# Kernel tuning notes

Hardware: AMD Instinct MI355X
Metric: run time of the kernel (lower is better)

The kernel has to match this reference:

```python
import jax, jax.numpy as jnp
import numpy as np

TOP_K = 8
CAP_FACTOR = 2  # expert capacity = CAP_FACTOR * T*K/E; generous so random routing drops ~nothing


def setup_inputs() -> dict:
    key = jax.random.key(0)
    ks = jax.random.split(key, 6)
    T, H, I, E = 4096, 1536, 768, 64
    return {
        "hidden_states": jax.random.normal(ks[0], (T, H), jnp.float32),
        "gate_w": jax.random.normal(ks[1], (E, H), jnp.float32) * 0.02,
        "routing_bias": jax.random.normal(ks[2], (E,), jnp.float32) * 0.02,
        "w_gate": jax.random.normal(ks[3], (E, I, H), jnp.float32) * 0.02,
        "w_up": jax.random.normal(ks[4], (E, I, H), jnp.float32) * 0.02,
        "w_down": jax.random.normal(ks[5], (E, H, I), jnp.float32) * 0.02,
        "num_global_tokens": 4096,
        "max_num_tokens_per_gpu": 4096,
    }


def _moe(hidden_states, gate_w, routing_bias, w_gate, w_up, w_down):
    T, H = hidden_states.shape
    E = gate_w.shape[0]
    K = TOP_K
    C = (CAP_FACTOR * T * K) // E  # expert capacity

    # router gemm in fp32 (matches fp32 gate / fp32_router_gemm)
    logits = hidden_states.astype(jnp.float32) @ gate_w.T           # [T, E]
    scores = jax.nn.sigmoid(logits)                                  # MiniMax2 sigmoid routing
    sel = scores + routing_bias[None, :]                             # correction bias only for selection
    _, idx = jax.lax.top_k(sel, K)                                   # [T, K]
    w = jnp.take_along_axis(scores, idx, axis=1)                     # weights from raw scores
    w = w / jnp.sum(w, axis=1, keepdims=True)                        # renormalize; routed_scaling_factor = 1.0

    # dispatch: position of each (token, k) row within its expert
    eids = idx.reshape(-1)                                           # [T*K]
    onehot = (eids[:, None] == jnp.arange(E)[None, :]).astype(jnp.int32)
    pos = jnp.take_along_axis(jnp.cumsum(onehot, axis=0) - 1, eids[:, None], axis=1)[:, 0]
    keep = pos < C
    posc = jnp.where(keep, pos, 0)
    x_rows = jnp.repeat(hidden_states, K, axis=0)                    # [T*K, H]
    xd = jnp.zeros((E, C, H), hidden_states.dtype).at[eids, posc].add(
        x_rows * keep[:, None].astype(hidden_states.dtype))         # [E, C, H]

    # grouped expert SwiGLU GEMMs
    g = jnp.einsum('ech,eih->eci', xd, w_gate)                       # [E, C, I]
    u = jnp.einsum('ech,eih->eci', xd, w_up)
    h = jax.nn.silu(g) * u
    y = jnp.einsum('eci,ehi->ech', h, w_down)                        # [E, C, H]

    # combine
    y_rows = y[eids, posc] * keep[:, None].astype(y.dtype)           # [T*K, H]
    out = jnp.sum(y_rows.reshape(T, K, H) * w.reshape(T, K, 1).astype(y.dtype), axis=1)
    return out.astype(hidden_states.dtype)


def reference(hidden_states, gate_w, routing_bias, w_gate, w_up, w_down,
              num_global_tokens, max_num_tokens_per_gpu):
    # num_global_tokens / max_num_tokens_per_gpu are distributed bookkeeping; no effect on math.
    return _moe(hidden_states, gate_w, routing_bias, w_gate, w_up, w_down)
```

## Files before the change

kernel.cpp:

```cpp
#include <hip/hip_runtime.h>
#include <hip/hip_bf16.h>
#include <math.h>

#define TTOK 4096
#define HD   1536
#define IDIM 768
#define NE   64
#define KSEL 8
#define CAP  1024
#define ECAP (NE * CAP)

typedef unsigned int uint32;
typedef __bf16 bf16;
typedef __attribute__((ext_vector_type(8))) __bf16 bf16x8;
typedef __attribute__((ext_vector_type(4))) __bf16 bf16x4;
typedef __attribute__((ext_vector_type(4))) float f32x4;

__global__ __launch_bounds__(256) void k_cast(const float* __restrict__ x, bf16* __restrict__ xb) {
    int i = (blockIdx.x * 256 + threadIdx.x) * 8;
    float4 a = *(const float4*)(x + i);
    float4 b = *(const float4*)(x + i + 4);
    bf16x8 o;
    o[0] = (bf16)a.x; o[1] = (bf16)a.y; o[2] = (bf16)a.z; o[3] = (bf16)a.w;
    o[4] = (bf16)b.x; o[5] = (bf16)b.y; o[6] = (bf16)b.z; o[7] = (bf16)b.w;
    *(bf16x8*)(xb + i) = o;
}

__global__ __launch_bounds__(256) void k_router(const float* __restrict__ x, const float* __restrict__ gw,
                                                double* __restrict__ logits) {
    __shared__ float Xt[8 * HD];
    int t0 = blockIdx.x * 8;
    int tid = threadIdx.x;
    {
        const float4* src = (const float4*)(x + (size_t)t0 * HD);
        float4* dst = (float4*)Xt;
        for (int u = tid; u < 8 * HD / 4; u += 256) dst[u] = src[u];
    }
    __syncthreads();
    int tr = tid >> 5;
    int er = (tid & 31) * 2;
    const float* xr = Xt + tr * HD;
    const float* g0 = gw + (size_t)er * HD;
    const float* g1 = g0 + HD;
    double c0 = 0.0, c1 = 0.0;
    for (int k = 0; k < HD; k += 4) {
        float4 a  = *(const float4*)(xr + k);
        float4 b0 = *(const float4*)(g0 + k);
        float4 b1 = *(const float4*)(g1 + k);
        c0 += (double)a.x * b0.x + (double)a.y * b0.y + (double)a.z * b0.z + (double)a.w * b0.w;
        c1 += (double)a.x * b1.x + (double)a.y * b1.y + (double)a.z * b1.z + (double)a.w * b1.w;
    }
    double* lp = logits + (size_t)(t0 + tr) * NE + er;
    lp[0] = c0; lp[1] = c1;
}

__global__ __launch_bounds__(64) void k_topk(const double* __restrict__ logits, const float* __restrict__ bias,
                                             float* __restrict__ wv, uint32* __restrict__ rowtok,
                                             uint32* __restrict__ tkof, int* __restrict__ cnt) {
    int t = blockIdx.x, lane = threadIdx.x;
    double lg = logits[(size_t)t * NE + lane];
    double sig = 1.0 / (1.0 + exp(-lg));
    double sel = sig + (double)bias[lane];
    double mysig = sig;
    double wsum = 0.0;
    int my_e = -1; double my_s = 0.0;
    for (int k = 0; k < KSEL; ++k) {
        double v = sel; int ei = lane;
        #pragma unroll
        for (int off = 32; off > 0; off >>= 1) {
            double ov = __shfl_down(v, off);
            int    oi = __shfl_down(ei, off);
            if (ov > v || (ov == v && oi < ei)) { v = ov; ei = oi; }
        }
        ei = __shfl(ei, 0);
        double sw = __shfl(mysig, ei);
        wsum += sw;
        if (lane == k) { my_e = ei; my_s = sw; }
        if (lane == ei) sel = -1.0e300;
    }
    if (lane < KSEL) {
        float w = (float)(my_s / wsum);
        int tk = t * KSEL + lane;
        int pos = atomicAdd(cnt + my_e, 1);
        if (pos < CAP) {
            rowtok[my_e * CAP + pos] = (uint32)t;
            tkof  [my_e * CAP + pos] = (uint32)tk;
            wv[tk] = w;
        } else {
            wv[tk] = 0.0f;
        }
    }
}

__global__ __launch_bounds__(256) void k_gemm1(const bf16* __restrict__ xb,
        const float* __restrict__ wg, const float* __restrict__ wu,
        const uint32* __restrict__ rowtok, const int* __restrict__ cnt,
        bf16* __restrict__ hc) {
    int id = blockIdx.x;
    int G  = ((id >> 6) << 3) | (id & 7);
    int mt = (id >> 3) & 7;
    int e  = G / 12, nt = G % 12;
    int n_rows = cnt[e];
    if (mt * 128 >= n_rows) return;

    __shared__ __align__(16) bf16 As[4 * 128 * 8];
    __shared__ __align__(16) bf16 Bg[4 * 64 * 8];
    __shared__ __align__(16) bf16 Bu[4 * 64 * 8];

    int tid = threadIdx.x;
    int am  = tid >> 2;
    int akc = tid & 3;
    int r0 = mt * 128 + am, r1 = r0 + 64;
    uint32 tok0 = (r0 < n_rows) ? rowtok[e * CAP + r0] : 0u;
    uint32 tok1 = (r1 < n_rows) ? rowtok[e * CAP + r1] : 0u;
    const bf16* a0p = xb + (size_t)tok0 * HD + akc * 8;
    const bf16* a1p = xb + (size_t)tok1 * HD + akc * 8;
    const float* wgp = wg + ((size_t)e * IDIM + nt * 64 + am) * HD + akc * 8;
    const float* wup = wu + ((size_t)e * IDIM + nt * 64 + am) * HD + akc * 8;

    int wave = tid >> 6, lane = tid & 63;
    int wm = wave & 1, wn = wave >> 1;
    int q = lane >> 4, r = lane & 15;

    f32x4 zero = {0.f, 0.f, 0.f, 0.f};
    f32x4 accg[4][2], accu[4][2];
    #pragma unroll
    for (int s = 0; s < 4; ++s)
        #pragma unroll
        for (int t2 = 0; t2 < 2; ++t2) { accg[s][t2] = zero; accu[s][t2] = zero; }

    bf16* asw0 = As + ((akc * 128) + am) * 8;
    bf16* asw1 = As + ((akc * 128) + am + 64) * 8;
    bf16* bgw  = Bg + ((akc * 64) + am) * 8;
    bf16* buw  = Bu + ((akc * 64) + am) * 8;

    for (int k0 = 0; k0 < HD; k0 += 32) {
        uint4 va0 = *(const uint4*)(a0p + k0);
        uint4 va1 = *(const uint4*)(a1p + k0);
        float4 gA = *(const float4*)(wgp + k0);
        float4 gB = *(const float4*)(wgp + k0 + 4);
        float4 uA = *(const float4*)(wup + k0);
        float4 uB = *(const float4*)(wup + k0 + 4);
        __syncthreads();
        *(uint4*)asw0 = va0;
        *(uint4*)asw1 = va1;
        bf16x8 pg, pu;
        pg[0]=(bf16)gA.x; pg[1]=(bf16)gA.y; pg[2]=(bf16)gA.z; pg[3]=(bf16)gA.w;
        pg[4]=(bf16)gB.x; pg[5]=(bf16)gB.y; pg[6]=(bf16)gB.z; pg[7]=(bf16)gB.w;
        pu[0]=(bf16)uA.x; pu[1]=(bf16)uA.y; pu[2]=(bf16)uA.z; pu[3]=(bf16)uA.w;
        pu[4]=(bf16)uB.x; pu[5]=(bf16)uB.y; pu[6]=(bf16)uB.z; pu[7]=(bf16)uB.w;
        *(bf16x8*)bgw = pg;
        *(bf16x8*)buw = pu;
        __syncthreads();
        bf16x8 af[4], bgf[2], buf2[2];
        #pragma unroll
        for (int s = 0; s < 4; ++s)
            af[s] = *(const bf16x8*)(As + (q * 128 + wm * 64 + s * 16 + r) * 8);
        #pragma unroll
        for (int t2 = 0; t2 < 2; ++t2) {
            bgf[t2]  = *(const bf16x8*)(Bg + (q * 64 + wn * 32 + t2 * 16 + r) * 8);
            buf2[t2] = *(const bf16x8*)(Bu + (q * 64 + wn * 32 + t2 * 16 + r) * 8);
        }
        #pragma unroll
        for (int s = 0; s < 4; ++s)
            #pragma unroll
            for (int t2 = 0; t2 < 2; ++t2) {
                accg[s][t2] = __builtin_amdgcn_mfma_f32_16x16x32_bf16(af[s], bgf[t2],  accg[s][t2], 0, 0, 0);
                accu[s][t2] = __builtin_amdgcn_mfma_f32_16x16x32_bf16(af[s], buf2[t2], accu[s][t2], 0, 0, 0);
            }
    }
    size_t rowbase = (size_t)e * CAP + mt * 128;
    #pragma unroll
    for (int s = 0; s < 4; ++s)
        #pragma unroll
        for (int t2 = 0; t2 < 2; ++t2)
            #pragma unroll
            for (int rg = 0; rg < 4; ++rg) {
                int row = wm * 64 + s * 16 + q * 4 + rg;
                int col = nt * 64 + wn * 32 + t2 * 16 + r;
                float g = accg[s][t2][rg], u = accu[s][t2][rg];
                float h = g / (1.f + __expf(-g)) * u;
                hc[(rowbase + row) * (size_t)IDIM + col] = (bf16)h;
            }
}

__global__ __launch_bounds__(256) void k_gemm2(const bf16* __restrict__ hc,
        const float* __restrict__ wd, const uint32* __restrict__ tkof,
        const int* __restrict__ cnt, bf16* __restrict__ yw) {
    int id = blockIdx.x;
    int G  = ((id >> 6) << 3) | (id & 7);
    int mt = (id >> 3) & 7;
    int e  = G / 12, nt = G % 12;
    int n_rows = cnt[e];
    if (mt * 128 >= n_rows) return;

    __shared__ __align__(16) bf16 As[4 * 128 * 8];
    __shared__ __align__(16) bf16 Bs[4 * 128 * 8];

    int tid = threadIdx.x;
    int am = tid >> 2, akc = tid & 3;
    const bf16*  a0p = hc + ((size_t)e * CAP + mt * 128 + am) * IDIM + akc * 8;
    const bf16*  a1p = a0p + (size_t)64 * IDIM;
    const float* b0p = wd + ((size_t)e * HD + nt * 128 + am) * IDIM + akc * 8;
    const float* b1p = b0p + (size_t)64 * IDIM;

    int wave = tid >> 6, lane = tid & 63;
    int wm = wave & 1, wn = wave >> 1;
    int q = lane >> 4, r = lane & 15;

    f32x4 zero = {0.f, 0.f, 0.f, 0.f};
    f32x4 acc[4][4];
    #pragma unroll
    for (int s = 0; s < 4; ++s)
        #pragma unroll
        for (int t2 = 0; t2 < 4; ++t2) acc[s][t2] = zero;

    bf16* asw0 = As + (akc * 128 + am) * 8;
    bf16* asw1 = As + (akc * 128 + am + 64) * 8;
    bf16* bsw0 = Bs + (akc * 128 + am) * 8;
    bf16* bsw1 = Bs + (akc * 128 + am + 64) * 8;

    for (int k0 = 0; k0 < IDIM; k0 += 32) {
        uint4 va0 = *(const uint4*)(a0p + k0);
        uint4 va1 = *(const uint4*)(a1p + k0);
        float4 cA = *(const float4*)(b0p + k0);
        float4 cB = *(const float4*)(b0p + k0 + 4);
        float4 dA = *(const float4*)(b1p + k0);
        float4 dB = *(const float4*)(b1p + k0 + 4);
        __syncthreads();
        *(uint4*)asw0 = va0;
        *(uint4*)asw1 = va1;
        bf16x8 p0, p1;
        p0[0]=(bf16)cA.x; p0[1]=(bf16)cA.y; p0[2]=(bf16)cA.z; p0[3]=(bf16)cA.w;
        p0[4]=(bf16)cB.x; p0[5]=(bf16)cB.y; p0[6]=(bf16)cB.z; p0[7]=(bf16)cB.w;
        p1[0]=(bf16)dA.x; p1[1]=(bf16)dA.y; p1[2]=(bf16)dA.z; p1[3]=(bf16)dA.w;
        p1[4]=(bf16)dB.x; p1[5]=(bf16)dB.y; p1[6]=(bf16)dB.z; p1[7]=(bf16)dB.w;
        *(bf16x8*)bsw0 = p0;
        *(bf16x8*)bsw1 = p1;
        __syncthreads();
        bf16x8 af[4], bf4[4];
        #pragma unroll
        for (int s = 0; s < 4; ++s)
            af[s] = *(const bf16x8*)(As + (q * 128 + wm * 64 + s * 16 + r) * 8);
        #pragma unroll
        for (int t2 = 0; t2 < 4; ++t2)
            bf4[t2] = *(const bf16x8*)(Bs + (q * 128 + wn * 64 + t2 * 16 + r) * 8);
        #pragma unroll
        for (int s = 0; s < 4; ++s)
            #pragma unroll
            for (int t2 = 0; t2 < 4; ++t2)
                acc[s][t2] = __builtin_amdgcn_mfma_f32_16x16x32_bf16(af[s], bf4[t2], acc[s][t2], 0, 0, 0);
    }
    uint32 tkx[4][4];
    #pragma unroll
    for (int s = 0; s < 4; ++s)
        #pragma unroll
        for (int rg = 0; rg < 4; ++rg) {
            int row = mt * 128 + wm * 64 + s * 16 + q * 4 + rg;
            tkx[s][rg] = (row < n_rows) ? tkof[e * CAP + row] : 0xFFFFFFFFu;
        }
    #pragma unroll
    for (int s = 0; s < 4; ++s)
        #pragma unroll
        for (int t2 = 0; t2 < 4; ++t2)
            #pragma unroll
            for (int rg = 0; rg < 4; ++rg) {
                if (tkx[s][rg] != 0xFFFFFFFFu) {
                    int col = nt * 128 + wn * 64 + t2 * 16 + r;
                    yw[(size_t)tkx[s][rg] * HD + col] = (bf16)acc[s][t2][rg];
                }
            }
}

__global__ __launch_bounds__(256) void k_combine(const bf16* __restrict__ yw,
        const float* __restrict__ wv, float* __restrict__ out) {
    int t = blockIdx.x, tid = threadIdx.x;
    __shared__ float w8[KSEL];
    if (tid < KSEL) w8[tid] = wv[t * KSEL + tid];
    __syncthreads();
    for (int c0 = tid * 4; c0 < HD; c0 += 1024) {
        float a0 = 0.f, a1 = 0.f, a2 = 0.f, a3 = 0.f;
        #pragma unroll
        for (int k = 0; k < KSEL; ++k) {
            bf16x4 v = *(const bf16x4*)(yw + ((size_t)(t * KSEL + k)) * HD + c0);
            float wk = w8[k];
            a0 += wk * (float)v[0];
            a1 += wk * (float)v[1];
            a2 += wk * (float)v[2];
            a3 += wk * (float)v[3];
        }
        float4 o = {a0, a1, a2, a3};
        *(float4*)(out + (size_t)t * HD + c0) = o;
    }
}

extern "C" void kernel_launch(void* const* d_in, const int* in_sizes, int n_in,
                              void* d_out, int out_size, void* d_ws, size_t ws_size,
                              hipStream_t stream) {
    const float* x  = (const float*)d_in[0];
    const float* gw = (const float*)d_in[1];
    const float* rb = (const float*)d_in[2];
    const float* wg = (const float*)d_in[3];
    const float* wu = (const float*)d_in[4];
    const float* wd = (const float*)d_in[5];
    float* out = (float*)d_out;

    char* ws = (char*)d_ws;
    size_t off = 0;
    auto alloc = [&](size_t bytes) -> void* {
        off = (off + 255) & ~(size_t)255;
        void* p = ws + off;
        off += bytes;
        return p;
    };
    bf16*   xb     = (bf16*)   alloc((size_t)TTOK * HD * 2);
    double* logits = (double*) alloc((size_t)TTOK * NE * 8);
    float*  wv     = (float*)  alloc((size_t)TTOK * KSEL * 4);
    uint32* rowtok = (uint32*) alloc((size_t)ECAP * 4);
    uint32* tkof   = (uint32*) alloc((size_t)ECAP * 4);
    int*    cnt    = (int*)    alloc(256);
    bf16*   hc     = (bf16*)   alloc((size_t)ECAP * IDIM * 2);
    bf16*   yw     = (bf16*)   alloc((size_t)TTOK * KSEL * HD * 2);
    (void)ws_size; (void)in_sizes; (void)n_in; (void)out_size; (void)rb;

    hipMemsetAsync(cnt, 0, 256, stream);
    k_cast   <<<TTOK * HD / 2048, 256, 0, stream>>>(x, xb);
    k_router <<<TTOK / 8,         256, 0, stream>>>(x, gw, logits);
    k_topk   <<<TTOK,             64,  0, stream>>>(logits, rb, wv, rowtok, tkof, cnt);
    k_gemm1  <<<6144,             256, 0, stream>>>(xb, wg, wu, rowtok, cnt, hc);
    k_gemm2  <<<6144,             256, 0, stream>>>(hc, wd, tkof, cnt, yw);
    k_combine<<<TTOK,             256, 0, stream>>>(yw, wv, out);
}
```

Before: 1.473 ms.

## Pre-cast expert weights to bf16 and stage GEMM tiles via global_load_lds

Adds a single cast kernel that converts all three expert weight tensors, plus the activations, to bf16 in workspace every call. Both grouped GEMMs then load bf16 tiles straight into LDS with global_load_lds in an MFMA-fragment-friendly layout, instead of loading fp32 into registers, converting and storing to LDS. This removes per-tile conversion and the register round-trip. The cost is an extra full pass over roughly 900MB of fp32 weights on every call, which may outweigh the savings, plus a second barrier per k-step. yw now aliases the wgb buffer.

```diff
diff --git a/kernel.cpp b/kernel.cpp
--- a/kernel.cpp
+++ b/kernel.cpp
@@ -16,14 +16,26 @@
 typedef __attribute__((ext_vector_type(4))) __bf16 bf16x4;
 typedef __attribute__((ext_vector_type(4))) float f32x4;
 
-__global__ __launch_bounds__(256) void k_cast(const float* __restrict__ x, bf16* __restrict__ xb) {
-    int i = (blockIdx.x * 256 + threadIdx.x) * 8;
-    float4 a = *(const float4*)(x + i);
-    float4 b = *(const float4*)(x + i + 4);
+#define GLD16(g, l) __builtin_amdgcn_global_load_lds( \
+    (const __attribute__((address_space(1))) void*)(g), \
+    (__attribute__((address_space(3))) void*)(l), 16, 0, 0)
+
+__global__ __launch_bounds__(256) void k_castall(const float* __restrict__ wg, const float* __restrict__ wu,
+        const float* __restrict__ wd, const float* __restrict__ x,
+        bf16* __restrict__ wgb, bf16* __restrict__ wub, bf16* __restrict__ wdb, bf16* __restrict__ xb) {
+    int b = blockIdx.x;
+    const float* src; bf16* dst; int base;
+    if      (b <  36864) { src = wg; dst = wgb; base = b; }
+    else if (b <  73728) { src = wu; dst = wub; base = b - 36864; }
+    else if (b < 110592) { src = wd; dst = wdb; base = b - 73728; }
+    else                 { src = x;  dst = xb;  base = b - 110592; }
+    size_t i = ((size_t)base * 256 + threadIdx.x) * 8;
+    float4 a = *(const float4*)(src + i);
+    float4 c = *(const float4*)(src + i + 4);
     bf16x8 o;
     o[0] = (bf16)a.x; o[1] = (bf16)a.y; o[2] = (bf16)a.z; o[3] = (bf16)a.w;
-    o[4] = (bf16)b.x; o[5] = (bf16)b.y; o[6] = (bf16)b.z; o[7] = (bf16)b.w;
-    *(bf16x8*)(xb + i) = o;
+    o[4] = (bf16)c.x; o[5] = (bf16)c.y; o[6] = (bf16)c.z; o[7] = (bf16)c.w;
+    *(bf16x8*)(dst + i) = o;
 }
 
 __global__ __launch_bounds__(256) void k_router(const float* __restrict__ x, const float* __restrict__ gw,
@@ -93,7 +105,7 @@
 }
 
 __global__ __launch_bounds__(256) void k_gemm1(const bf16* __restrict__ xb,
-        const float* __restrict__ wg, const float* __restrict__ wu,
+        const bf16* __restrict__ wgb, const bf16* __restrict__ wub,
         const uint32* __restrict__ rowtok, const int* __restrict__ cnt,
         bf16* __restrict__ hc) {
     int id = blockIdx.x;
@@ -103,24 +115,29 @@
     int n_rows = cnt[e];
     if (mt * 128 >= n_rows) return;
 
-    __shared__ __align__(16) bf16 As[4 * 128 * 8];
-    __shared__ __align__(16) bf16 Bg[4 * 64 * 8];
-    __shared__ __align__(16) bf16 Bu[4 * 64 * 8];
-
-    int tid = threadIdx.x;
-    int am  = tid >> 2;
-    int akc = tid & 3;
-    int r0 = mt * 128 + am, r1 = r0 + 64;
+    __shared__ __align__(16) bf16 As[128 * 32];
+    __shared__ __align__(16) bf16 Bg[64 * 32];
+    __shared__ __align__(16) bf16 Bu[64 * 32];
+
+    int tid = threadIdx.x, wave = tid >> 6, lane = tid & 63;
+    int kc = lane >> 4, mr = lane & 15;
+
+    int g0 = wave * 2, g1 = g0 + 1;
+    int r0 = mt * 128 + g0 * 16 + mr, r1 = mt * 128 + g1 * 16 + mr;
     uint32 tok0 = (r0 < n_rows) ? rowtok[e * CAP + r0] : 0u;
     uint32 tok1 = (r1 < n_rows) ? rowtok[e * CAP + r1] : 0u;
-    const bf16* a0p = xb + (size_t)tok0 * HD + akc * 8;
-    const bf16* a1p = xb + (size_t)tok1 * HD + akc * 8;
-    const float* wgp = wg + ((size_t)e * IDIM + nt * 64 + am) * HD + akc * 8;
-    const float* wup = wu + ((size_t)e * IDIM + nt * 64 + am) * HD + akc * 8;
-
-    int wave = tid >> 6, lane = tid & 63;
+    const bf16* ga0 = xb + (size_t)tok0 * HD + kc * 8;
+    const bf16* ga1 = xb + (size_t)tok1 * HD + kc * 8;
+    const bf16* gbg = wgb + ((size_t)e * IDIM + nt * 64 + wave * 16 + mr) * HD + kc * 8;
+    const bf16* gbu = wub + ((size_t)e * IDIM + nt * 64 + wave * 16 + mr) * HD + kc * 8;
+
+    bf16* lA0 = As + g0 * 512;
+    bf16* lA1 = As + g1 * 512;
+    bf16* lBg = Bg + wave * 512;
+    bf16* lBu = Bu + wave * 512;
+
     int wm = wave & 1, wn = wave >> 1;
-    int q = lane >> 4, r = lane & 15;
+    int r = lane & 15, q = lane >> 4;
 
     f32x4 zero = {0.f, 0.f, 0.f, 0.f};
     f32x4 accg[4][2], accu[4][2];
@@ -129,37 +146,20 @@
         #pragma unroll
         for (int t2 = 0; t2 < 2; ++t2) { accg[s][t2] = zero; accu[s][t2] = zero; }
 
-    bf16* asw0 = As + ((akc * 128) + am) * 8;
-    bf16* asw1 = As + ((akc * 128) + am + 64) * 8;
-    bf16* bgw  = Bg + ((akc * 64) + am) * 8;
-    bf16* buw  = Bu + ((akc * 64) + am) * 8;
-
     for (int k0 = 0; k0 < HD; k0 += 32) {
-        uint4 va0 = *(const uint4*)(a0p + k0);
-        uint4 va1 = *(const uint4*)(a1p + k0);
-        float4 gA = *(const float4*)(wgp + k0);
-        float4 gB = *(const float4*)(wgp + k0 + 4);
-        float4 uA = *(const float4*)(wup + k0);
-        float4 uB = *(const float4*)(wup + k0 + 4);
-        __syncthreads();
-        *(uint4*)asw0 = va0;
-        *(uint4*)asw1 = va1;
-        bf16x8 pg, pu;
-        pg[0]=(bf16)gA.x; pg[1]=(bf16)gA.y; pg[2]=(bf16)gA.z; pg[3]=(bf16)gA.w;
-        pg[4]=(bf16)gB.x; pg[5]=(bf16)gB.y; pg[6]=(bf16)gB.z; pg[7]=(bf16)gB.w;
-        pu[0]=(bf16)uA.x; pu[1]=(bf16)uA.y; pu[2]=(bf16)uA.z; pu[3]=(bf16)uA.w;
-        pu[4]=(bf16)uB.x; pu[5]=(bf16)uB.y; pu[6]=(bf16)uB.z; pu[7]=(bf16)uB.w;
-        *(bf16x8*)bgw = pg;
-        *(bf16x8*)buw = pu;
+        GLD16(ga0 + k0, lA0);
+        GLD16(ga1 + k0, lA1);
+        GLD16(gbg + k0, lBg);
+        GLD16(gbu + k0, lBu);
         __syncthreads();
         bf16x8 af[4], bgf[2], buf2[2];
         #pragma unroll
         for (int s = 0; s < 4; ++s)
-            af[s] = *(const bf16x8*)(As + (q * 128 + wm * 64 + s * 16 + r) * 8);
+            af[s] = *(const bf16x8*)(As + (wm * 4 + s) * 512 + lane * 8);
         #pragma unroll
         for (int t2 = 0; t2 < 2; ++t2) {
-            bgf[t2]  = *(const bf16x8*)(Bg + (q * 64 + wn * 32 + t2 * 16 + r) * 8);
-            buf2[t2] = *(const bf16x8*)(Bu + (q * 64 + wn * 32 + t2 * 16 + r) * 8);
+            bgf[t2]  = *(const bf16x8*)(Bg + (wn * 2 + t2) * 512 + lane * 8);
+            buf2[t2] = *(const bf16x8*)(Bu + (wn * 2 + t2) * 512 + lane * 8);
         }
         #pragma unroll
         for (int s = 0; s < 4; ++s)
@@ -168,6 +168,7 @@
                 accg[s][t2] = __builtin_amdgcn_mfma_f32_16x16x32_bf16(af[s], bgf[t2],  accg[s][t2], 0, 0, 0);
                 accu[s][t2] = __builtin_amdgcn_mfma_f32_16x16x32_bf16(af[s], buf2[t2], accu[s][t2], 0, 0, 0);
             }
+        __syncthreads();
     }
     size_t rowbase = (size_t)e * CAP + mt * 128;
     #pragma unroll
@@ -185,7 +186,7 @@
 }
 
 __global__ __launch_bounds__(256) void k_gemm2(const bf16* __restrict__ hc,
-        const float* __restrict__ wd, const uint32* __restrict__ tkof,
+        const bf16* __restrict__ wdb, const uint32* __restrict__ tkof,
         const int* __restrict__ cnt, bf16* __restrict__ yw) {
     int id = blockIdx.x;
     int G  = ((id >> 6) << 3) | (id & 7);
@@ -194,19 +195,25 @@
     int n_rows = cnt[e];
     if (mt * 128 >= n_rows) return;
 
-    __shared__ __align__(16) bf16 As[4 * 128 * 8];
-    __shared__ __align__(16) bf16 Bs[4 * 128 * 8];
-
-    int tid = threadIdx.x;
-    int am = tid >> 2, akc = tid & 3;
-    const bf16*  a0p = hc + ((size_t)e * CAP + mt * 128 + am) * IDIM + akc * 8;
-    const bf16*  a1p = a0p + (size_t)64 * IDIM;
-    const float* b0p = wd + ((size_t)e * HD + nt * 128 + am) * IDIM + akc * 8;
-    const float* b1p = b0p + (size_t)64 * IDIM;
-
-    int wave = tid >> 6, lane = tid & 63;
+    __shared__ __align__(16) bf16 As[128 * 32];
+    __shared__ __align__(16) bf16 Bs[128 * 32];
+
+    int tid = threadIdx.x, wave = tid >> 6, lane = tid & 63;
+    int kc = lane >> 4, mr = lane & 15;
+
+    int g0 = wave * 2, g1 = g0 + 1;
+    const bf16* ga0 = hc + ((size_t)e * CAP + mt * 128 + g0 * 16 + mr) * IDIM + kc * 8;
+    const bf16* ga1 = hc + ((size_t)e * CAP + mt * 128 + g1 * 16 + mr) * IDIM + kc * 8;
+    const bf16* gb0 = wdb + ((size_t)e * HD + nt * 128 + g0 * 16 + mr) * IDIM + kc * 8;
+    const bf16* gb1 = wdb + ((size_t)e * HD + nt * 128 + g1 * 16 + mr) * IDIM + kc * 8;
+
+    bf16* lA0 = As + g0 * 512;
+    bf16* lA1 = As + g1 * 512;
+    bf16* lB0 = Bs + g0 * 512;
+    bf16* lB1 = Bs + g1 * 512;
+
     int wm = wave & 1, wn = wave >> 1;
-    int q = lane >> 4, r = lane & 15;
+    int r = lane & 15, q = lane >> 4;
 
     f32x4 zero = {0.f, 0.f, 0.f, 0.f};
     f32x4 acc[4][4];
@@ -215,41 +222,25 @@
         #pragma unroll
         for (int t2 = 0; t2 < 4; ++t2) acc[s][t2] = zero;
 
-    bf16* asw0 = As + (akc * 128 + am) * 8;
-    bf16* asw1 = As + (akc * 128 + am + 64) * 8;
-    bf16* bsw0 = Bs + (akc * 128 + am) * 8;
-    bf16* bsw1 = Bs + (akc * 128 + am + 64) * 8;
-
     for (int k0 = 0; k0 < IDIM; k0 += 32) {
-        uint4 va0 = *(const uint4*)(a0p + k0);
-        uint4 va1 = *(const uint4*)(a1p + k0);
-        float4 cA = *(const float4*)(b0p + k0);
-        float4 cB = *(const float4*)(b0p + k0 + 4);
-        float4 dA = *(const float4*)(b1p + k0);
-        float4 dB = *(const float4*)(b1p + k0 + 4);
-        __syncthreads();
-        *(uint4*)asw0 = va0;
-        *(uint4*)asw1 = va1;
-        bf16x8 p0, p1;
-        p0[0]=(bf16)cA.x; p0[1]=(bf16)cA.y; p0[2]=(bf16)cA.z; p0[3]=(bf16)cA.w;
-        p0[4]=(bf16)cB.x; p0[5]=(bf16)cB.y; p0[6]=(bf16)cB.z; p0[7]=(bf16)cB.w;
-        p1[0]=(bf16)dA.x; p1[1]=(bf16)dA.y; p1[2]=(bf16)dA.z; p1[3]=(bf16)dA.w;
-        p1[4]=(bf16)dB.x; p1[5]=(bf16)dB.y; p1[6]=(bf16)dB.z; p1[7]=(bf16)dB.w;
-        *(bf16x8*)bsw0 = p0;
-        *(bf16x8*)bsw1 = p1;
+        GLD16(ga0 + k0, lA0);
+        GLD16(ga1 + k0, lA1);
+        GLD16(gb0 + k0, lB0);
+        GLD16(gb1 + k0, lB1);
         __syncthreads();
         bf16x8 af[4], bf4[4];
         #pragma unroll
         for (int s = 0; s < 4; ++s)
-            af[s] = *(const bf16x8*)(As + (q * 128 + wm * 64 + s * 16 + r) * 8);
+            af[s] = *(const bf16x8*)(As + (wm * 4 + s) * 512 + lane * 8);
         #pragma unroll
         for (int t2 = 0; t2 < 4; ++t2)
-            bf4[t2] = *(const bf16x8*)(Bs + (q * 128 + wn * 64 + t2 * 16 + r) * 8);
+            bf4[t2] = *(const bf16x8*)(Bs + (wn * 4 + t2) * 512 + lane * 8);
         #pragma unroll
         for (int s = 0; s < 4; ++s)
             #pragma unroll
             for (int t2 = 0; t2 < 4; ++t2)
                 acc[s][t2] = __builtin_amdgcn_mfma_f32_16x16x32_bf16(af[s], bf4[t2], acc[s][t2], 0, 0, 0);
+        __syncthreads();
     }
     uint32 tkx[4][4];
     #pragma unroll
@@ -313,21 +304,25 @@
         off += bytes;
         return p;
     };
+    const size_t WELEM = (size_t)NE * IDIM * HD;
     bf16*   xb     = (bf16*)   alloc((size_t)TTOK * HD * 2);
     double* logits = (double*) alloc((size_t)TTOK * NE * 8);
     float*  wv     = (float*)  alloc((size_t)TTOK * KSEL * 4);
     uint32* rowtok = (uint32*) alloc((size_t)ECAP * 4);
     uint32* tkof   = (uint32*) alloc((size_t)ECAP * 4);
     int*    cnt    = (int*)    alloc(256);
+    bf16*   wdb    = (bf16*)   alloc(WELEM * 2);
     bf16*   hc     = (bf16*)   alloc((size_t)ECAP * IDIM * 2);
-    bf16*   yw     = (bf16*)   alloc((size_t)TTOK * KSEL * HD * 2);
-    (void)ws_size; (void)in_sizes; (void)n_in; (void)out_size; (void)rb;
+    bf16*   wgb    = (bf16*)   alloc(WELEM * 2);
+    bf16*   wub    = (bf16*)   alloc(WELEM * 2);
+    bf16*   yw     = wgb;
+    (void)ws_size; (void)in_sizes; (void)n_in; (void)out_size;
 
     hipMemsetAsync(cnt, 0, 256, stream);
-    k_cast   <<<TTOK * HD / 2048, 256, 0, stream>>>(x, xb);
-    k_router <<<TTOK / 8,         256, 0, stream>>>(x, gw, logits);
-    k_topk   <<<TTOK,             64,  0, stream>>>(logits, rb, wv, rowtok, tkof, cnt);
-    k_gemm1  <<<6144,             256, 0, stream>>>(xb, wg, wu, rowtok, cnt, hc);
-    k_gemm2  <<<6144,             256, 0, stream>>>(hc, wd, tkof, cnt, yw);
-    k_combine<<<TTOK,             256, 0, stream>>>(yw, wv, out);
-}
+    k_castall<<<113664,   256, 0, stream>>>(wg, wu, wd, x, wgb, wub, wdb, xb);
+    k_router <<<TTOK / 8, 256, 0, stream>>>(x, gw, logits);
+    k_topk   <<<TTOK,     64,  0, stream>>>(logits, rb, wv, rowtok, tkof, cnt);
+    k_gemm1  <<<6144,     256, 0, stream>>>(xb, wgb, wub, rowtok, cnt, hc);
+    k_gemm2  <<<6144,     256, 0, stream>>>(hc, wdb, tkof, cnt, yw);
+    k_combine<<<TTOK,     256, 0, stream>>>(yw, wv, out);
+}
```

Result: slower. 1.710 ms (+16.1%).
